# Optimization experiments

Hardware: AMD Instinct MI355X
Metric: run time of the kernel (lower is better)

## Reference

```python
import jax, jax.numpy as jnp
import numpy as np

EPS = 1e-08
BN_EPS = 1e-05

def _bn(x, gamma, beta):
    # BatchNorm1d training mode: biased variance over batch axis
    mean = x.mean(axis=0)
    var = x.var(axis=0)
    return (x - mean) / jnp.sqrt(var + BN_EPS) * gamma + beta

def setup_inputs() -> dict:
    key = jax.random.key(0)
    ks = jax.random.split(key, 16)
    N, E, H = 100000, 1600000, 64
    D = H // 4  # 16
    def lin(k, fin, fout):
        lim = 1.0 / np.sqrt(fin)
        kw, kb = jax.random.split(k)
        W = jax.random.uniform(kw, (fin, fout), jnp.float32, -lim, lim)
        b = jax.random.uniform(kb, (fout,), jnp.float32, -lim, lim)
        return W, b
    W1, b1 = lin(ks[0], 8, H)
    W2, b2 = lin(ks[1], H, H // 2)
    W3, b3 = lin(ks[2], H // 2, D)
    Wp, bp = lin(ks[3], D, D)
    return {
        "coords": jax.random.normal(ks[4], (N, 3), jnp.float32),
        "normals": jax.random.normal(ks[5], (N, 3), jnp.float32),
        "curvatures": jax.random.normal(ks[6], (N, 4), jnp.float32),
        "edge_index": jax.random.randint(ks[7], (2, E), 0, N, jnp.int64),
        "W1": W1, "b1": b1, "W2": W2, "b2": b2, "W3": W3, "b3": b3,
        "Wp": Wp, "bp": bp,
        "bn_edge_g": jnp.ones((D,), jnp.float32), "bn_edge_b": jnp.zeros((D,), jnp.float32),
        "bn_node_g": jnp.ones((D,), jnp.float32), "bn_node_b": jnp.zeros((D,), jnp.float32),
    }

def reference(coords, normals, curvatures, edge_index, W1, b1, W2, b2, W3, b3,
              Wp, bp, bn_edge_g, bn_edge_b, bn_node_g, bn_node_b):
    N = coords.shape[0]
    row, col = edge_index[0], edge_index[1]
    # gather per-edge geometry
    delta = coords[col] - coords[row]                                  # [E,3]
    n_row, n_col = normals[row], normals[col]                          # [E,3]
    normal_dot = (n_row * n_col).sum(-1, keepdims=True)                # [E,1]
    delta_norm = jnp.linalg.norm(delta, axis=-1, keepdims=True) + EPS
    cos_row = jnp.clip((n_row * delta).sum(-1, keepdims=True) / delta_norm, -1 + EPS, 1 - EPS)
    cos_col = jnp.clip((n_col * delta).sum(-1, keepdims=True) / delta_norm, -1 + EPS, 1 - EPS)
    curv_diff = curvatures[col, :2] - curvatures[row, :2]              # [E,2]
    ef = jnp.concatenate([delta, normal_dot, cos_row, cos_col, curv_diff], axis=-1)  # [E,8]
    # edge MLP (exact GELU as in torch nn.GELU default)
    h = jax.nn.gelu(ef @ W1 + b1, approximate=False)
    h = jax.nn.gelu(h @ W2 + b2, approximate=False)
    h = h @ W3 + b3                                                    # [E,16]
    h = _bn(h, bn_edge_g, bn_edge_b)
    # scatter-add to both endpoints
    D = h.shape[-1]
    node_feat = jnp.zeros((N, D), h.dtype).at[row].add(h).at[col].add(h)
    ones = jnp.ones(row.shape, h.dtype)
    degree = jnp.zeros((N,), h.dtype).at[row].add(ones).at[col].add(ones)
    degree = jnp.clip(degree, 1.0)
    node_feat = node_feat / degree[:, None]
    node_feat = node_feat @ Wp + bp
    node_feat = _bn(node_feat, bn_node_g, bn_node_b)
    return node_feat
```

## Files before the change

kernel.cpp:

```cpp
#include <hip/hip_runtime.h>
#include <hip/hip_fp16.h>
#include <math.h>

#define EPSF 1e-8f
#define BN_EPSF 1e-5f

typedef __attribute__((ext_vector_type(8))) short short8;
typedef __attribute__((ext_vector_type(4))) float float4v;

static __device__ __forceinline__ short f2bf(float f) {
    unsigned u = __float_as_uint(f);
    unsigned r = (u + 0x7FFFu + ((u >> 16) & 1u)) >> 16;
    return (short)r;
}

static __device__ __forceinline__ unsigned short f2h(float f) {
    return __half_as_ushort(__float2half(f));
}

__device__ __forceinline__ float gelu_fast(float x) {
    const float z = fabsf(x) * 0.70710678118654752440f;
    const float t = __builtin_amdgcn_rcpf(1.0f + 0.3275911f * z);
    float p = 1.061405429f;
    p = p * t - 1.453152027f;
    p = p * t + 1.421413741f;
    p = p * t - 0.284496736f;
    p = p * t + 0.254829592f;
    p = p * t;
    const float e = __builtin_amdgcn_exp2f(z * z * -1.44269504088896340736f);
    float erfv = 1.0f - p * e;
    erfv = copysignf(erfv, x);
    return 0.5f * x * (1.0f + erfv);
}

static __device__ __forceinline__ void atomic_pk_add_f16(void* p, unsigned data) {
    const unsigned long long addr = (unsigned long long)p;
    asm volatile("global_atomic_pk_add_f16 %0, %1, off" :: "v"(addr), "v"(data) : "memory");
}

__global__ __launch_bounds__(256) void pack_nodes_zero(
    const float* __restrict__ coords, const float* __restrict__ normals,
    const float* __restrict__ curv, float* __restrict__ pk,
    unsigned short* __restrict__ acch, int N)
{
    const int n = blockIdx.x * blockDim.x + threadIdx.x;
    if (n < N) {
        float4 a, b;
        a.x = coords[3*n+0]; a.y = coords[3*n+1]; a.z = coords[3*n+2];
        a.w = normals[3*n+0];
        b.x = normals[3*n+1]; b.y = normals[3*n+2];
        b.z = curv[4*n+0];    b.w = curv[4*n+1];
        float4* o = (float4*)(pk + (size_t)n * 8);
        o[0] = a; o[1] = b;
        uint4* ab = (uint4*)(acch + (size_t)n * 32);
        const uint4 z = make_uint4(0,0,0,0);
        ab[0] = z; ab[1] = z; ab[2] = z; ab[3] = z;
    }
}

__global__ __launch_bounds__(256, 4) void edge_kernel(
    const float* __restrict__ pk, const int* __restrict__ eidx,
    const float* __restrict__ W1, const float* __restrict__ b1,
    const float* __restrict__ W2, const float* __restrict__ b2,
    const float* __restrict__ W3, const float* __restrict__ b3,
    unsigned short* __restrict__ acch,
    float* __restrict__ epartial, int E)
{
    __shared__ short w1t[64][32];
    __shared__ short w2t[32][64];
    __shared__ short w3t[16][32];
    __shared__ short ef_lds[4][64][8];
    __shared__ short h1_lds[4][16][72];
    __shared__ short h2_lds[4][16][40];
    __shared__ unsigned short hbuf16[256][18];
    __shared__ int   nidbuf[512];
    __shared__ float redbuf[4][32];

    const int t    = threadIdx.x;
    const int wv   = t >> 6;
    const int ln   = t & 63;
    const int qd   = ln >> 4;
    const int m    = ln & 15;
    const int base = blockIdx.x * 256;

    for (int idx = t; idx < 64*32; idx += 256) {
        const int n = idx >> 5, k = idx & 31;
        w1t[n][k] = (k < 8) ? f2bf(W1[k*64 + n]) : (short)0;
    }
    for (int idx = t; idx < 32*64; idx += 256) {
        const int n = idx >> 6, k = idx & 63;
        w2t[n][k] = f2bf(W2[k*32 + n]);
    }
    for (int idx = t; idx < 16*32; idx += 256) {
        const int n = idx >> 5, k = idx & 31;
        w3t[n][k] = f2bf(W3[k*16 + n]);
    }

    const int e = base + t;
    float ef[8];
    #pragma unroll
    for (int i = 0; i < 8; ++i) ef[i] = 0.0f;
    int r = -1, c = -1;
    if (e < E) {
        r = eidx[e];
        c = eidx[E + e];
        const float4 r0 = *(const float4*)(pk + (size_t)r * 8);
        const float4 r1 = *(const float4*)(pk + (size_t)r * 8 + 4);
        const float4 c0 = *(const float4*)(pk + (size_t)c * 8);
        const float4 c1 = *(const float4*)(pk + (size_t)c * 8 + 4);

        const float dx = c0.x - r0.x;
        const float dy = c0.y - r0.y;
        const float dz = c0.z - r0.z;
        const float nrx = r0.w, nry = r1.x, nrz = r1.y;
        const float ncx = c0.w, ncy = c1.x, ncz = c1.y;
        const float ndot = nrx*ncx + nry*ncy + nrz*ncz;
        const float dn = sqrtf(dx*dx + dy*dy + dz*dz) + EPSF;
        const float inv_dn = 1.0f / dn;
        float cr = (nrx*dx + nry*dy + nrz*dz) * inv_dn;
        float cc = (ncx*dx + ncy*dy + ncz*dz) * inv_dn;
        const float lo = -1.0f + EPSF, hi = 1.0f - EPSF;
        cr = fminf(fmaxf(cr, lo), hi);
        cc = fminf(fmaxf(cc, lo), hi);
        ef[0] = dx; ef[1] = dy; ef[2] = dz; ef[3] = ndot;
        ef[4] = cr; ef[5] = cc; ef[6] = c1.z - r1.z; ef[7] = c1.w - r1.w;
    }
    nidbuf[t]       = r;
    nidbuf[256 + t] = c;

    {
        int p[4];
        #pragma unroll
        for (int i = 0; i < 4; ++i) {
            p[i] = ((unsigned short)f2bf(ef[2*i])) |
                   (((unsigned)(unsigned short)f2bf(ef[2*i+1])) << 16);
        }
        *(int4*)&ef_lds[wv][ln][0] = make_int4(p[0], p[1], p[2], p[3]);
    }

    __syncthreads();

    short8 fw1[4], fw2[2][2], fw3;
    #pragma unroll
    for (int nt = 0; nt < 4; ++nt)
        fw1[nt] = *(const short8*)&w1t[nt*16 + m][qd*8];
    #pragma unroll
    for (int ks = 0; ks < 2; ++ks)
        #pragma unroll
        for (int nt = 0; nt < 2; ++nt)
            fw2[ks][nt] = *(const short8*)&w2t[nt*16 + m][ks*32 + qd*8];
    fw3 = *(const short8*)&w3t[m][qd*8];

    float bias1[4], bias2[2];
    #pragma unroll
    for (int nt = 0; nt < 4; ++nt) bias1[nt] = b1[nt*16 + m];
    #pragma unroll
    for (int nt = 0; nt < 2; ++nt) bias2[nt] = b2[nt*16 + m];
    const float bias3 = b3[m];

    float ssum = 0.0f, qsum = 0.0f;

    for (int tl = 0; tl < 4; ++tl) {
        short8 a1 = {0,0,0,0,0,0,0,0};
        if (qd == 0) a1 = *(const short8*)&ef_lds[wv][tl*16 + m][0];
        float4v c1[4];
        #pragma unroll
        for (int nt = 0; nt < 4; ++nt) {
            c1[nt] = (float4v){bias1[nt], bias1[nt], bias1[nt], bias1[nt]};
            c1[nt] = __builtin_amdgcn_mfma_f32_16x16x32_bf16(a1, fw1[nt], c1[nt], 0, 0, 0);
        }
        #pragma unroll
        for (int nt = 0; nt < 4; ++nt)
            #pragma unroll
            for (int rg = 0; rg < 4; ++rg)
                h1_lds[wv][qd*4 + rg][nt*16 + m] = f2bf(gelu_fast(c1[nt][rg]));

        float4v c2[2];
        #pragma unroll
        for (int nt = 0; nt < 2; ++nt)
            c2[nt] = (float4v){bias2[nt], bias2[nt], bias2[nt], bias2[nt]};
        #pragma unroll
        for (int ks = 0; ks < 2; ++ks) {
            const short8 a2 = *(const short8*)&h1_lds[wv][m][ks*32 + qd*8];
            #pragma unroll
            for (int nt = 0; nt < 2; ++nt)
                c2[nt] = __builtin_amdgcn_mfma_f32_16x16x32_bf16(a2, fw2[ks][nt], c2[nt], 0, 0, 0);
        }
        #pragma unroll
        for (int nt = 0; nt < 2; ++nt)
            #pragma unroll
            for (int rg = 0; rg < 4; ++rg)
                h2_lds[wv][qd*4 + rg][nt*16 + m] = f2bf(gelu_fast(c2[nt][rg]));

        const short8 a3 = *(const short8*)&h2_lds[wv][m][qd*8];
        float4v c3 = (float4v){bias3, bias3, bias3, bias3};
        c3 = __builtin_amdgcn_mfma_f32_16x16x32_bf16(a3, fw3, c3, 0, 0, 0);

        const int ebase = wv*64 + tl*16 + qd*4;
        #pragma unroll
        for (int rg = 0; rg < 4; ++rg) {
            const int ebl = ebase + rg;
            float v = c3[rg];
            hbuf16[ebl][m] = f2h(v);
            if (nidbuf[ebl] < 0) v = 0.0f;
            ssum += v;
            qsum += v * v;
        }
    }

    {
        const int jid  = ln / 9;
        const int role = ln - jid * 9;
        #pragma unroll 1
        for (int it = 0; it < 19; ++it) {
            const int j = it * 7 + jid;
            if (jid < 7 && j < 128) {
                const int slot = wv * 64 + (j >> 1);
                const int side = j & 1;
                const int nid  = nidbuf[side * 256 + slot];
                if (nid >= 0) {
                    const unsigned data = (role == 8)
                        ? 0x3C00u
                        : *(const unsigned*)&hbuf16[slot][role * 2];
                    atomic_pk_add_f16(acch + (size_t)nid * 32 + role * 2, data);
                }
            }
        }
    }

    ssum += __shfl_xor(ssum, 16); ssum += __shfl_xor(ssum, 32);
    qsum += __shfl_xor(qsum, 16); qsum += __shfl_xor(qsum, 32);
    if (qd == 0) redbuf[wv][m]      = ssum;
    if (qd == 1) redbuf[wv][16 + m] = qsum;
    __syncthreads();

    if (t < 32) {
        epartial[(size_t)blockIdx.x * 32 + t] =
            redbuf[0][t] + redbuf[1][t] + redbuf[2][t] + redbuf[3][t];
    }
}

__global__ __launch_bounds__(256) void reduce_partials(
    const float* __restrict__ p, int nblk, float* __restrict__ stats)
{
    const int k = blockIdx.x;
    float s = 0.0f;
    for (int i = threadIdx.x; i < nblk; i += blockDim.x) s += p[(size_t)i * 32 + k];
    #pragma unroll
    for (int o = 32; o > 0; o >>= 1) s += __shfl_xor(s, o);
    __shared__ float w[4];
    if ((threadIdx.x & 63) == 0) w[threadIdx.x >> 6] = s;
    __syncthreads();
    if (threadIdx.x == 0) stats[k] = w[0] + w[1] + w[2] + w[3];
}

__global__ void finalize_bn(const float* __restrict__ stats,
                            const float* __restrict__ g, const float* __restrict__ b,
                            float cnt_inv, float* __restrict__ coef)
{
    const int j = threadIdx.x;
    if (j < 16) {
        const float mean = stats[j] * cnt_inv;
        const float var  = stats[16 + j] * cnt_inv - mean * mean;
        const float inv  = rsqrtf(var + BN_EPSF);
        const float a    = g[j] * inv;
        coef[j]      = a;
        coef[16 + j] = b[j] - mean * a;
    }
}

__global__ __launch_bounds__(256) void node_kernel(
    const unsigned short* __restrict__ acch,
    const float* __restrict__ ecoef,
    const float* __restrict__ Wp, const float* __restrict__ bp,
    float* __restrict__ y, float* __restrict__ npartial, int N)
{
    __shared__ float redbuf[4][32];
    const int t = threadIdx.x;
    const int n = blockIdx.x * 256 + t;

    float yv[16];
    #pragma unroll
    for (int j = 0; j < 16; ++j) yv[j] = 0.0f;

    if (n < N) {
        const unsigned short* row = acch + (size_t)n * 32;
        const uint4 u0 = *(const uint4*)row;
        const uint4 u1 = *(const uint4*)(row + 8);
        const float d  = __half2float(__ushort_as_half(row[16]));
        const float inv = 1.0f / fmaxf(d, 1.0f);
        unsigned w[8] = {u0.x, u0.y, u0.z, u0.w, u1.x, u1.y, u1.z, u1.w};
        float x[16];
        #pragma unroll
        for (int q = 0; q < 8; ++q) {
            x[2*q]   = __half2float(__ushort_as_half((unsigned short)(w[q] & 0xFFFFu)));
            x[2*q+1] = __half2float(__ushort_as_half((unsigned short)(w[q] >> 16)));
        }
        #pragma unroll
        for (int j = 0; j < 16; ++j)
            x[j] = (ecoef[j] * x[j] + ecoef[16 + j] * d) * inv;

        #pragma unroll
        for (int j = 0; j < 16; ++j) yv[j] = bp[j];
        #pragma unroll
        for (int i = 0; i < 16; ++i) {
            const float v = x[i];
            #pragma unroll
            for (int j = 0; j < 16; ++j) yv[j] += v * Wp[i*16 + j];
        }
        float4* yrow = (float4*)(y + (size_t)n * 16);
        #pragma unroll
        for (int q = 0; q < 4; ++q) {
            float4 o;
            o.x = yv[4*q+0]; o.y = yv[4*q+1]; o.z = yv[4*q+2]; o.w = yv[4*q+3];
            yrow[q] = o;
        }
    }

    const int wave = t >> 6;
    #pragma unroll
    for (int j = 0; j < 16; ++j) {
        float s = yv[j];
        float q = yv[j] * yv[j];
        #pragma unroll
        for (int o = 32; o > 0; o >>= 1) {
            s += __shfl_xor(s, o);
            q += __shfl_xor(q, o);
        }
        if ((t & 63) == 0) {
            redbuf[wave][j]      = s;
            redbuf[wave][16 + j] = q;
        }
    }
    __syncthreads();
    if (t < 32) {
        npartial[(size_t)blockIdx.x * 32 + t] =
            redbuf[0][t] + redbuf[1][t] + redbuf[2][t] + redbuf[3][t];
    }
}

__global__ __launch_bounds__(256) void final_kernel(
    float* __restrict__ out, const float* __restrict__ ncoef, int total)
{
    const int i = (blockIdx.x * blockDim.x + threadIdx.x) * 4;
    if (i < total) {
        const float4 v = *(const float4*)(out + i);
        const int j = i & 15;
        const float4 a = *(const float4*)(ncoef + j);
        const float4 c = *(const float4*)(ncoef + 16 + j);
        float4 o;
        o.x = v.x * a.x + c.x;
        o.y = v.y * a.y + c.y;
        o.z = v.z * a.z + c.z;
        o.w = v.w * a.w + c.w;
        *(float4*)(out + i) = o;
    }
}

extern "C" void kernel_launch(void* const* d_in, const int* in_sizes, int n_in,
                              void* d_out, int out_size, void* d_ws, size_t ws_size,
                              hipStream_t stream) {
    const float* coords = (const float*)d_in[0];
    const float* normals = (const float*)d_in[1];
    const float* curv = (const float*)d_in[2];
    const int*   eidx = (const int*)d_in[3];
    const float* W1 = (const float*)d_in[4];
    const float* b1 = (const float*)d_in[5];
    const float* W2 = (const float*)d_in[6];
    const float* b2 = (const float*)d_in[7];
    const float* W3 = (const float*)d_in[8];
    const float* b3 = (const float*)d_in[9];
    const float* Wp = (const float*)d_in[10];
    const float* bp = (const float*)d_in[11];
    const float* bn_edge_g = (const float*)d_in[12];
    const float* bn_edge_b = (const float*)d_in[13];
    const float* bn_node_g = (const float*)d_in[14];
    const float* bn_node_b = (const float*)d_in[15];

    const int N = in_sizes[0] / 3;
    const int E = in_sizes[3] / 2;

    const int eblocks = (E + 255) / 256;
    const int nblocks = (N + 255) / 256;

    float* ws = (float*)d_ws;
    unsigned short* acch = (unsigned short*)ws;
    float* ecoef    = ws + (size_t)N * 16;
    float* ncoef    = ecoef + 32;
    float* estats   = ncoef + 32;
    float* nstats   = estats + 32;
    float* epartial = nstats + 32;
    float* npartial = epartial + (size_t)eblocks * 32;
    float* pk       = npartial + (size_t)nblocks * 32;

    pack_nodes_zero<<<nblocks, 256, 0, stream>>>(coords, normals, curv, pk, acch, N);

    edge_kernel<<<eblocks, 256, 0, stream>>>(
        pk, eidx, W1, b1, W2, b2, W3, b3, acch, epartial, E);

    reduce_partials<<<32, 256, 0, stream>>>(epartial, eblocks, estats);
    finalize_bn<<<1, 64, 0, stream>>>(estats, bn_edge_g, bn_edge_b, 1.0f / (float)E, ecoef);

    node_kernel<<<nblocks, 256, 0, stream>>>(
        acch, ecoef, Wp, bp, (float*)d_out, npartial, N);

    reduce_partials<<<32, 256, 0, stream>>>(npartial, nblocks, nstats);
    finalize_bn<<<1, 64, 0, stream>>>(nstats, bn_node_g, bn_node_b, 1.0f / (float)N, ncoef);

    const int total = N * 16;
    final_kernel<<<(total / 4 + 255) / 256, 256, 0, stream>>>((float*)d_out, ncoef, total);
}
```

Before: 332.3 us.

## Fuse node BN into node kernel via grid-wide atomic barrier; merge reduce+finalize

Merges the partial-reduction and BN-finalize launches into one kernel for the edge stats. It also fuses the node projection, the node BN statistics reduction and the final normalization into a single kernel, using an atomic counter as a grid-wide barrier. This removes several small launches and the write-then-reread of the output. The barrier assumes all 391 blocks are co-resident, which holds on this GPU but risks deadlock otherwise.

```diff
diff --git a/kernel.cpp b/kernel.cpp
--- a/kernel.cpp
+++ b/kernel.cpp
@@ -41,9 +41,10 @@
 __global__ __launch_bounds__(256) void pack_nodes_zero(
     const float* __restrict__ coords, const float* __restrict__ normals,
     const float* __restrict__ curv, float* __restrict__ pk,
-    unsigned short* __restrict__ acch, int N)
+    unsigned short* __restrict__ acch, unsigned* __restrict__ cnt, int N)
 {
     const int n = blockIdx.x * blockDim.x + threadIdx.x;
+    if (n == 0) *cnt = 0u;
     if (n < N) {
         float4 a, b;
         a.x = coords[3*n+0]; a.y = coords[3*n+1]; a.z = coords[3*n+2];
@@ -240,28 +241,31 @@
     }
 }
 
-__global__ __launch_bounds__(256) void reduce_partials(
-    const float* __restrict__ p, int nblk, float* __restrict__ stats)
+__global__ __launch_bounds__(256) void reduce_finalize(
+    const float* __restrict__ p, int nblk,
+    const float* __restrict__ g, const float* __restrict__ b,
+    float cnt_inv, float* __restrict__ coef)
 {
-    const int k = blockIdx.x;
-    float s = 0.0f;
-    for (int i = threadIdx.x; i < nblk; i += blockDim.x) s += p[(size_t)i * 32 + k];
-    #pragma unroll
-    for (int o = 32; o > 0; o >>= 1) s += __shfl_xor(s, o);
-    __shared__ float w[4];
-    if ((threadIdx.x & 63) == 0) w[threadIdx.x >> 6] = s;
-    __syncthreads();
-    if (threadIdx.x == 0) stats[k] = w[0] + w[1] + w[2] + w[3];
-}
-
-__global__ void finalize_bn(const float* __restrict__ stats,
-                            const float* __restrict__ g, const float* __restrict__ b,
-                            float cnt_inv, float* __restrict__ coef)
-{
-    const int j = threadIdx.x;
-    if (j < 16) {
-        const float mean = stats[j] * cnt_inv;
-        const float var  = stats[16 + j] * cnt_inv - mean * mean;
+    const int j = blockIdx.x;
+    const int t = threadIdx.x;
+    float s = 0.0f, q = 0.0f;
+    for (int i = t; i < nblk; i += 256) {
+        s += p[(size_t)i * 32 + j];
+        q += p[(size_t)i * 32 + 16 + j];
+    }
+    #pragma unroll
+    for (int o = 32; o > 0; o >>= 1) {
+        s += __shfl_xor(s, o);
+        q += __shfl_xor(q, o);
+    }
+    __shared__ float wsm[8];
+    if ((t & 63) == 0) { wsm[t >> 6] = s; wsm[4 + (t >> 6)] = q; }
+    __syncthreads();
+    if (t == 0) {
+        const float su = wsm[0] + wsm[1] + wsm[2] + wsm[3];
+        const float sq = wsm[4] + wsm[5] + wsm[6] + wsm[7];
+        const float mean = su * cnt_inv;
+        const float var  = sq * cnt_inv - mean * mean;
         const float inv  = rsqrtf(var + BN_EPSF);
         const float a    = g[j] * inv;
         coef[j]      = a;
@@ -269,15 +273,21 @@
     }
 }
 
-__global__ __launch_bounds__(256) void node_kernel(
+__global__ __launch_bounds__(256) void node_final(
     const unsigned short* __restrict__ acch,
     const float* __restrict__ ecoef,
     const float* __restrict__ Wp, const float* __restrict__ bp,
-    float* __restrict__ y, float* __restrict__ npartial, int N)
+    const float* __restrict__ gn, const float* __restrict__ bn,
+    float* __restrict__ out, float* __restrict__ npartial,
+    unsigned* __restrict__ cnt, int N)
 {
     __shared__ float redbuf[4][32];
-    const int t = threadIdx.x;
-    const int n = blockIdx.x * 256 + t;
+    __shared__ float sb[8][32];
+    __shared__ float coefs[32];
+
+    const int t    = threadIdx.x;
+    const int n    = blockIdx.x * 256 + t;
+    const int nblk = gridDim.x;
 
     float yv[16];
     #pragma unroll
@@ -308,13 +318,6 @@
             #pragma unroll
             for (int j = 0; j < 16; ++j) yv[j] += v * Wp[i*16 + j];
         }
-        float4* yrow = (float4*)(y + (size_t)n * 16);
-        #pragma unroll
-        for (int q = 0; q < 4; ++q) {
-            float4 o;
-            o.x = yv[4*q+0]; o.y = yv[4*q+1]; o.z = yv[4*q+2]; o.w = yv[4*q+3];
-            yrow[q] = o;
-        }
     }
 
     const int wave = t >> 6;
@@ -334,26 +337,57 @@
     }
     __syncthreads();
     if (t < 32) {
-        npartial[(size_t)blockIdx.x * 32 + t] =
-            redbuf[0][t] + redbuf[1][t] + redbuf[2][t] + redbuf[3][t];
-    }
-}
-
-__global__ __launch_bounds__(256) void final_kernel(
-    float* __restrict__ out, const float* __restrict__ ncoef, int total)
-{
-    const int i = (blockIdx.x * blockDim.x + threadIdx.x) * 4;
-    if (i < total) {
-        const float4 v = *(const float4*)(out + i);
-        const int j = i & 15;
-        const float4 a = *(const float4*)(ncoef + j);
-        const float4 c = *(const float4*)(ncoef + 16 + j);
-        float4 o;
-        o.x = v.x * a.x + c.x;
-        o.y = v.y * a.y + c.y;
-        o.z = v.z * a.z + c.z;
-        o.w = v.w * a.w + c.w;
-        *(float4*)(out + i) = o;
+        const float v = redbuf[0][t] + redbuf[1][t] + redbuf[2][t] + redbuf[3][t];
+        __hip_atomic_store(&npartial[(size_t)blockIdx.x * 32 + t], v,
+                           __ATOMIC_RELEASE, __HIP_MEMORY_SCOPE_AGENT);
+    }
+    __syncthreads();
+
+    if (t == 0) {
+        __hip_atomic_fetch_add(cnt, 1u, __ATOMIC_ACQ_REL, __HIP_MEMORY_SCOPE_AGENT);
+        unsigned v;
+        do {
+            v = __hip_atomic_load(cnt, __ATOMIC_ACQUIRE, __HIP_MEMORY_SCOPE_AGENT);
+            if (v < (unsigned)nblk) __builtin_amdgcn_s_sleep(2);
+        } while (v < (unsigned)nblk);
+    }
+    __syncthreads();
+
+    {
+        const int k  = t & 31;
+        const int r0 = t >> 5;
+        float s = 0.0f;
+        for (int i = r0; i < nblk; i += 8)
+            s += __hip_atomic_load(&npartial[(size_t)i * 32 + k],
+                                   __ATOMIC_RELAXED, __HIP_MEMORY_SCOPE_AGENT);
+        sb[r0][k] = s;
+    }
+    __syncthreads();
+    if (t < 16) {
+        float su = 0.0f, sq = 0.0f;
+        #pragma unroll
+        for (int j = 0; j < 8; ++j) { su += sb[j][t]; sq += sb[j][16 + t]; }
+        const float cnt_inv = 1.0f / (float)N;
+        const float mean = su * cnt_inv;
+        const float var  = sq * cnt_inv - mean * mean;
+        const float inv  = rsqrtf(var + BN_EPSF);
+        const float a    = gn[t] * inv;
+        coefs[t]      = a;
+        coefs[16 + t] = bn[t] - mean * a;
+    }
+    __syncthreads();
+
+    if (n < N) {
+        float4* orow = (float4*)(out + (size_t)n * 16);
+        #pragma unroll
+        for (int q4 = 0; q4 < 4; ++q4) {
+            float4 o;
+            o.x = yv[4*q4+0] * coefs[4*q4+0] + coefs[16 + 4*q4+0];
+            o.y = yv[4*q4+1] * coefs[4*q4+1] + coefs[16 + 4*q4+1];
+            o.z = yv[4*q4+2] * coefs[4*q4+2] + coefs[16 + 4*q4+2];
+            o.w = yv[4*q4+3] * coefs[4*q4+3] + coefs[16 + 4*q4+3];
+            orow[q4] = o;
+        }
     }
 }
 
@@ -386,27 +420,20 @@
     float* ws = (float*)d_ws;
     unsigned short* acch = (unsigned short*)ws;
     float* ecoef    = ws + (size_t)N * 16;
-    float* ncoef    = ecoef + 32;
-    float* estats   = ncoef + 32;
-    float* nstats   = estats + 32;
-    float* epartial = nstats + 32;
+    unsigned* cnt   = (unsigned*)(ecoef + 32);
+    float* epartial = ecoef + 40;
     float* npartial = epartial + (size_t)eblocks * 32;
     float* pk       = npartial + (size_t)nblocks * 32;
 
-    pack_nodes_zero<<<nblocks, 256, 0, stream>>>(coords, normals, curv, pk, acch, N);
+    pack_nodes_zero<<<nblocks, 256, 0, stream>>>(coords, normals, curv, pk, acch, cnt, N);
 
     edge_kernel<<<eblocks, 256, 0, stream>>>(
         pk, eidx, W1, b1, W2, b2, W3, b3, acch, epartial, E);
 
-    reduce_partials<<<32, 256, 0, stream>>>(epartial, eblocks, estats);
-    finalize_bn<<<1, 64, 0, stream>>>(estats, bn_edge_g, bn_edge_b, 1.0f / (float)E, ecoef);
-
-    node_kernel<<<nblocks, 256, 0, stream>>>(
-        acch, ecoef, Wp, bp, (float*)d_out, npartial, N);
-
-    reduce_partials<<<32, 256, 0, stream>>>(npartial, nblocks, nstats);
-    finalize_bn<<<1, 64, 0, stream>>>(nstats, bn_node_g, bn_node_b, 1.0f / (float)N, ncoef);
-
-    const int total = N * 16;
-    final_kernel<<<(total / 4 + 255) / 256, 256, 0, stream>>>((float*)d_out, ncoef, total);
-}
+    reduce_finalize<<<16, 256, 0, stream>>>(epartial, eblocks, bn_edge_g, bn_edge_b,
+                                            1.0f / (float)E, ecoef);
+
+    node_final<<<nblocks, 256, 0, stream>>>(
+        acch, ecoef, Wp, bp, bn_node_g, bn_node_b,
+        (float*)d_out, npartial, cnt, N);
+}
```

Measured after the change: 365.2 us. 1.1x slower.
